# Performance work log

Measured on AMD Instinct MI355X. Metric: run time of the kernel, lower is better.

## Reference

```python
import jax, jax.numpy as jnp
import numpy as np

B, N, D, H = 4, 4096, 1024, 16
DH = D // H          # per-head dim = 64
M = 256              # number of random features
KEPS = 1e-3          # performer kernel epsilon
LNEPS = 1e-5


def setup_inputs() -> dict:
    key = jax.random.key(0)
    ks = jax.random.split(key, 16)
    s = 0.02
    return {
        "src": jax.random.normal(ks[0], (B, N, D), jnp.float32),
        "Wq": s * jax.random.normal(ks[1], (D, D), jnp.float32),
        "Wk": s * jax.random.normal(ks[2], (D, D), jnp.float32),
        "Wv": s * jax.random.normal(ks[3], (D, D), jnp.float32),
        "Wout": s * jax.random.normal(ks[4], (D, D), jnp.float32),
        "b_out": jnp.zeros((D,), jnp.float32),
        "proj": jax.random.normal(ks[5], (M, DH), jnp.float32),
        "g1": jnp.ones((D,), jnp.float32),
        "beta1": jnp.zeros((D,), jnp.float32),
        "W1": s * jax.random.normal(ks[6], (2048, D), jnp.float32),
        "b1": jnp.zeros((2048,), jnp.float32),
        "W2": s * jax.random.normal(ks[7], (D, 2048), jnp.float32),
        "b2": jnp.zeros((D,), jnp.float32),
        "g2": jnp.ones((D,), jnp.float32),
        "beta2": jnp.zeros((D,), jnp.float32),
    }


def _layernorm(x, g, b):
    mu = x.mean(-1, keepdims=True)
    var = ((x - mu) ** 2).mean(-1, keepdims=True)
    return (x - mu) * jax.lax.rsqrt(var + LNEPS) * g + b


def _softmax_kernel(x, proj, is_query):
    # FAVOR+ positive softmax kernel feature map (performer_pytorch)
    dn = DH ** -0.25           # data normalizer d^{-1/4}
    ratio = M ** -0.5
    data_dash = jnp.einsum('bhnd,md->bhnm', x * dn, proj)
    diag = (x ** 2).sum(-1) * 0.5 * dn * dn            # [b,h,n]
    if is_query:
        stab = data_dash.max(-1, keepdims=True)
    else:
        stab = data_dash.max()
    return ratio * (jnp.exp(data_dash - diag[..., None] - stab) + KEPS)


def reference(src, Wq, Wk, Wv, Wout, b_out, proj, g1, beta1, W1, b1, W2, b2, g2, beta2):
    # ---- Performer self-attention (FAVOR+, non-causal) ----
    def split_heads(x):
        return x.reshape(B, N, H, DH).transpose(0, 2, 1, 3)  # [b,h,n,dh]

    q = split_heads(src @ Wq.T)
    k = split_heads(src @ Wk.T)
    v = split_heads(src @ Wv.T)

    qp = _softmax_kernel(q, proj, is_query=True)   # [b,h,n,m]
    kp = _softmax_kernel(k, proj, is_query=False)  # [b,h,n,m]

    k_sum = kp.sum(-2)                                        # [b,h,m]
    d_inv = 1.0 / jnp.einsum('bhnm,bhm->bhn', qp, k_sum)      # [b,h,n]
    context = jnp.einsum('bhnm,bhnd->bhmd', kp, v)            # [b,h,m,dh]
    attn = jnp.einsum('bhnm,bhmd->bhnd', qp, context) * d_inv[..., None]

    attn = attn.transpose(0, 2, 1, 3).reshape(B, N, D)
    src2 = attn @ Wout.T + b_out

    # ---- residual + norm + FFN (dropout = identity at eval) ----
    x = _layernorm(src + src2, g1, beta1)
    ff = (jax.nn.gelu(x @ W1.T + b1, approximate=False)) @ W2.T + b2
    return _layernorm(x + ff, g2, beta2)
```

## Files before the change

kernel.cpp:

```cpp
#include <hip/hip_runtime.h>

#define DEVI __device__ __forceinline__

using u16 = unsigned short;
using u32 = unsigned int;
using u64 = unsigned long long;

typedef __bf16 bf16x8 __attribute__((ext_vector_type(8)));
typedef float  f32x4  __attribute__((ext_vector_type(4)));

constexpr int BB = 4, NN = 4096, DD = 1024, HH = 16, DH = 64, MF = 256;
constexpr int RT = BB * NN;
constexpr int QKVS = 3072;
constexpr float DN    = 0.35355339059327373f;
constexpr float RATIO = 0.0625f;
constexpr float DIAGC = 0.0625f;
constexpr float KEPSC = 1e-3f;

DEVI u16 f2bf(float f) {
  u32 u = __float_as_uint(f);
  u32 r = u + 0x7fffu + ((u >> 16) & 1u);
  return (u16)(r >> 16);
}
DEVI float bf2f(u16 u) { return __uint_as_float(((u32)u) << 16); }

typedef void __attribute__((address_space(1)))* gas1;
typedef void __attribute__((address_space(3)))* las3;
DEVI void gload_lds16(const void* g, void* l) {
  __builtin_amdgcn_global_load_lds((gas1)(u64)g, (las3)(u32)(u64)l, 16, 0, 0);
}

DEVI bf16x8 ldswz(const u16* base, int row, int kbyte) {
  int p = (row << 7) + kbyte;
  p ^= (row & 7) << 4;
  return *(const bf16x8*)((const char*)base + p);
}

__global__ void cast_kernel(const float* __restrict__ in, u16* __restrict__ out, int n4) {
  int i = blockIdx.x * 256 + threadIdx.x;
  int stride = gridDim.x * 256;
  for (; i < n4; i += stride) {
    float4 v = ((const float4*)in)[i];
    ushort4 o; o.x = f2bf(v.x); o.y = f2bf(v.y); o.z = f2bf(v.z); o.w = f2bf(v.w);
    ((ushort4*)out)[i] = o;
  }
}

__global__ void cast_weights_kernel(
    const float* __restrict__ Wq, const float* __restrict__ Wk,
    const float* __restrict__ Wv, const float* __restrict__ Wout,
    const float* __restrict__ W1, const float* __restrict__ W2,
    const float* __restrict__ proj,
    u16* __restrict__ wqkvb, u16* __restrict__ wob,
    u16* __restrict__ w1b, u16* __restrict__ w2b, u16* __restrict__ projb)
{
  constexpr int TOT = 2101248;
  int i = blockIdx.x * 256 + threadIdx.x;
  const int stride = gridDim.x * 256;
  for (; i < TOT; i += stride) {
    const float* s; u16* d; int loc; float sc = 1.0f;
    if (i < 1048576) {
      int seg = i >> 18; loc = i & 262143;
      s = (seg == 0) ? Wq : (seg == 1) ? Wk : (seg == 2) ? Wv : Wout;
      d = (seg < 3) ? (wqkvb + seg * 1048576) : wob;
    } else if (i < 1572864) { loc = i - 1048576; s = W1; d = w1b; }
    else if (i < 2097152)   { loc = i - 1572864; s = W2; d = w2b; }
    else                    { loc = i - 2097152; s = proj; d = projb; sc = DN; }
    float4 v = ((const float4*)s)[loc];
    ushort4 o; o.x = f2bf(v.x * sc); o.y = f2bf(v.y * sc); o.z = f2bf(v.z * sc); o.w = f2bf(v.w * sc);
    ((ushort4*)d)[loc] = o;
  }
}

template <int EPI>
__global__ __launch_bounds__(512, 4) void gemm_bt(
    const u16* __restrict__ A, int lda, const u16* __restrict__ Bm,
    u16* __restrict__ Cb, const float* __restrict__ bias,
    int Ncols, int K)
{
  __shared__ __align__(16) u16 sA[256 * 64];
  __shared__ __align__(16) u16 sB[128 * 64];
  const int tid = threadIdx.x, lane = tid & 63;
  const int wv = tid >> 6, wr = wv >> 1, wc = wv & 1;

  const int gx = gridDim.x;
  const int wg = blockIdx.y * gx + blockIdx.x;
  const int cpx = (gx * gridDim.y) >> 3;
  const int swz = (wg & 7) * cpx + (wg >> 3);
  const int bn = swz % gx, bm = swz / gx;

  f32x4 acc[4][4] = {};

  int rowS[4], colS[4], ldsb[4];
#pragma unroll
  for (int it = 0; it < 4; ++it) {
    int p = (it * 512 + tid) * 16;
    ldsb[it] = (it * 512 + (tid & ~63)) * 16;
    int sp = p ^ (((p >> 7) & 7) << 4);
    rowS[it] = sp >> 7;
    colS[it] = (sp >> 1) & 63;
  }
  const size_t baseA = (size_t)bm * 256, baseB = (size_t)bn * 128;

  for (int kt = 0; kt < K; kt += 64) {
#pragma unroll
    for (int it = 0; it < 4; ++it)
      gload_lds16(A + (baseA + rowS[it]) * lda + kt + colS[it], (char*)sA + ldsb[it]);
#pragma unroll
    for (int it = 0; it < 2; ++it)
      gload_lds16(Bm + (baseB + rowS[it]) * K + kt + colS[it], (char*)sB + ldsb[it]);
    __syncthreads();
#pragma unroll
    for (int kk = 0; kk < 2; ++kk) {
      const int kbyte = kk * 64 + ((lane >> 4) << 4);
      bf16x8 a[4], b[4];
#pragma unroll
      for (int i = 0; i < 4; ++i) a[i] = ldswz(sA, wr * 64 + i * 16 + (lane & 15), kbyte);
#pragma unroll
      for (int i = 0; i < 4; ++i) b[i] = ldswz(sB, wc * 64 + i * 16 + (lane & 15), kbyte);
#pragma unroll
      for (int i = 0; i < 4; ++i)
#pragma unroll
        for (int j = 0; j < 4; ++j)
          acc[i][j] = __builtin_amdgcn_mfma_f32_16x16x32_bf16(a[i], b[j], acc[i][j], 0, 0, 0);
    }
    __syncthreads();
  }

#pragma unroll
  for (int i = 0; i < 4; ++i) {
    const int gr0 = bm * 256 + wr * 64 + i * 16 + ((lane >> 4) << 2);
#pragma unroll
    for (int j = 0; j < 4; ++j) {
      const int gc = bn * 128 + wc * 64 + j * 16 + (lane & 15);
#pragma unroll
      for (int r = 0; r < 4; ++r) {
        const size_t o = (size_t)(gr0 + r) * Ncols + gc;
        const float v = acc[i][j][r];
        if constexpr (EPI == 0) {
          Cb[o] = f2bf(v);
        } else if constexpr (EPI == 2) {
          float t = v + bias[gc];
          Cb[o] = f2bf(0.5f * t * (1.0f + erff(t * 0.70710678118654752f)));
        } else {
          Cb[o] = f2bf(v + bias[gc]);
        }
      }
    }
  }
}

__global__ __launch_bounds__(256) void kmax_kernel(
    const u16* __restrict__ qkvb, const u16* __restrict__ projb, float* __restrict__ pmax)
{
  __shared__ __align__(16) u16 sX[64 * 72];
  __shared__ float sred[4];
  const int tid = threadIdx.x, lane = tid & 63, wv = tid >> 6;
  const int bh = blockIdx.x, b = bh >> 4, h = bh & 15;
  const int n0 = blockIdx.y * 64;

  for (int i = tid; i < 512; i += 256) {
    int r = i >> 3, c8 = (i & 7) << 3;
    uint4 v = *(const uint4*)(qkvb + ((size_t)(b * NN + n0 + r)) * QKVS + 1024 + h * DH + c8);
    *(uint4*)&sX[r * 72 + c8] = v;
  }
  __syncthreads();

  f32x4 dacc[16] = {};
#pragma unroll
  for (int kk = 0; kk < 2; ++kk) {
    const int ko = kk * 32 + ((lane >> 4) << 3);
    bf16x8 a = *(const bf16x8*)&sX[(wv * 16 + (lane & 15)) * 72 + ko];
#pragma unroll
    for (int f = 0; f < 16; ++f) {
      bf16x8 bb = *(const bf16x8*)(projb + (f * 16 + (lane & 15)) * 64 + ko);
      dacc[f] = __builtin_amdgcn_mfma_f32_16x16x32_bf16(a, bb, dacc[f], 0, 0, 0);
    }
  }
  float mx = -1e30f;
#pragma unroll
  for (int f = 0; f < 16; ++f)
#pragma unroll
    for (int r = 0; r < 4; ++r) mx = fmaxf(mx, dacc[f][r]);
#pragma unroll
  for (int m = 1; m < 64; m <<= 1) mx = fmaxf(mx, __shfl_xor(mx, m));
  if (lane == 0) sred[wv] = mx;
  __syncthreads();
  if (tid == 0)
    pmax[blockIdx.y * gridDim.x + blockIdx.x] =
        fmaxf(fmaxf(sred[0], sred[1]), fmaxf(sred[2], sred[3]));
}

__global__ __launch_bounds__(256) void reduce_max_kernel(
    const float* __restrict__ pmax, float* __restrict__ stab)
{
  const int tid = threadIdx.x;
  float mx = -1e30f;
#pragma unroll
  for (int i = 0; i < 16; ++i) mx = fmaxf(mx, pmax[i * 256 + tid]);
#pragma unroll
  for (int m = 1; m < 64; m <<= 1) mx = fmaxf(mx, __shfl_xor(mx, m));
  __shared__ float sred[4];
  if ((tid & 63) == 0) sred[tid >> 6] = mx;
  __syncthreads();
  if (tid == 0)
    stab[0] = fmaxf(fmaxf(sred[0], sred[1]), fmaxf(sred[2], sred[3]));
}

__global__ __launch_bounds__(256, 1) void kctx_kernel(
    const u16* __restrict__ qkvb, const u16* __restrict__ projb,
    const float* __restrict__ stab_p,
    float* __restrict__ ctxT, float* __restrict__ ksum)
{
  __shared__ __align__(16) u16 sX[64 * 72];
  __shared__ __align__(16) u16 sVT[64 * 72];
  __shared__ __align__(16) u16 sKpT[256 * 72];
  __shared__ float sDiag[64];
  const int tid = threadIdx.x, lane = tid & 63, wv = tid >> 6;
  const int bh = blockIdx.x, b = bh >> 4, h = bh & 15;
  const int sl = blockIdx.y;
  const float stab = stab_p[0];

  f32x4 cacc[16] = {};
  float ksacc[16] = {};
  const int row_base = wv * 16 + ((lane >> 4) << 2);

  for (int t = 0; t < 8; ++t) {
    const int n0 = sl * 512 + t * 64;
    if (t) __syncthreads();
    for (int i = tid; i < 512; i += 256) {
      int r = i >> 3, c8 = (i & 7) << 3;
      size_t g = ((size_t)(b * NN + n0 + r)) * QKVS + h * DH + c8;
      uint4 xv = *(const uint4*)(qkvb + g + 1024);
      *(uint4*)&sX[r * 72 + c8] = xv;
      uint4 vv = *(const uint4*)(qkvb + g + 2048);
      const u16* pv = (const u16*)&vv;
#pragma unroll
      for (int j = 0; j < 8; ++j) sVT[(c8 + j) * 72 + r] = pv[j];
    }
    __syncthreads();
    {
      int r = tid >> 2, qq = tid & 3;
      float s = 0;
#pragma unroll
      for (int j = 0; j < 16; ++j) { float x = bf2f(sX[r * 72 + qq * 16 + j]); s += x * x; }
      s += __shfl_xor(s, 1); s += __shfl_xor(s, 2);
      if (qq == 0) sDiag[r] = DIAGC * s;
    }
    f32x4 dacc[16] = {};
#pragma unroll
    for (int kk = 0; kk < 2; ++kk) {
      const int ko = kk * 32 + ((lane >> 4) << 3);
      bf16x8 a = *(const bf16x8*)&sX[(wv * 16 + (lane & 15)) * 72 + ko];
#pragma unroll
      for (int f = 0; f < 16; ++f) {
        bf16x8 bb = *(const bf16x8*)(projb + (f * 16 + (lane & 15)) * 64 + ko);
        dacc[f] = __builtin_amdgcn_mfma_f32_16x16x32_bf16(a, bb, dacc[f], 0, 0, 0);
      }
    }
    __syncthreads();
#pragma unroll
    for (int f = 0; f < 16; ++f) {
      float kvv[4]; float cs = 0;
#pragma unroll
      for (int r = 0; r < 4; ++r) {
        float val = RATIO * (__expf(dacc[f][r] - sDiag[row_base + r] - stab) + KEPSC);
        kvv[r] = val; cs += val;
      }
      cs += __shfl_xor(cs, 16); cs += __shfl_xor(cs, 32);
      ksacc[f] += cs;
      ushort4 pk; pk.x = f2bf(kvv[0]); pk.y = f2bf(kvv[1]); pk.z = f2bf(kvv[2]); pk.w = f2bf(kvv[3]);
      *(ushort4*)&sKpT[(f * 16 + (lane & 15)) * 72 + row_base] = pk;
    }
    __syncthreads();
#pragma unroll
    for (int kk = 0; kk < 2; ++kk) {
      const int ko = kk * 32 + ((lane >> 4) << 3);
      bf16x8 a = *(const bf16x8*)&sVT[(wv * 16 + (lane & 15)) * 72 + ko];
#pragma unroll
      for (int f = 0; f < 16; ++f) {
        bf16x8 bb = *(const bf16x8*)&sKpT[(f * 16 + (lane & 15)) * 72 + ko];
        cacc[f] = __builtin_amdgcn_mfma_f32_16x16x32_bf16(a, bb, cacc[f], 0, 0, 0);
      }
    }
  }
#pragma unroll
  for (int f = 0; f < 16; ++f) {
    const int m = f * 16 + (lane & 15);
#pragma unroll
    for (int r = 0; r < 4; ++r)
      atomicAdd(&ctxT[((size_t)bh * 64 + row_base + r) * 256 + m], cacc[f][r]);
  }
  if (lane < 16) {
#pragma unroll
    for (int f = 0; f < 16; ++f) atomicAdd(&ksum[bh * 256 + f * 16 + lane], ksacc[f]);
  }
}

__global__ __launch_bounds__(256) void ctxfin_kernel(
    const float* __restrict__ ctxT, u16* __restrict__ ctxb)
{
  const int i = blockIdx.x * 256 + threadIdx.x;
  float4 v = ((const float4*)ctxT)[i];
  ushort4 o; o.x = f2bf(v.x); o.y = f2bf(v.y); o.z = f2bf(v.z); o.w = f2bf(v.w);
  ((ushort4*)ctxb)[i] = o;
}

__global__ __launch_bounds__(256, 2) void qattn_kernel(
    u16* qkvb, const u16* __restrict__ projb,
    const u16* __restrict__ ctxb, const float* __restrict__ ksum)
{
  __shared__ __align__(16) u16 sCtx[64 * 256];
  __shared__ __align__(16) u16 sX[64 * 72];
  __shared__ __align__(16) u16 sQp[64 * 264];
  __shared__ float sKsum[256];
  __shared__ float sDiag[64];
  __shared__ float sDinv[64];
  const int tid = threadIdx.x, lane = tid & 63, wv = tid >> 6;
  const int bh = blockIdx.x, b = bh >> 4, h = bh & 15;

  {
    const char* cbase = (const char*)(ctxb + (size_t)bh * 16384);
#pragma unroll
    for (int it = 0; it < 8; ++it) {
      int p = (it * 256 + tid) * 16;
      int ldsb = (it * 256 + (tid & ~63)) * 16;
      int q = p ^ (((p >> 9) & 7) << 4);
      gload_lds16(cbase + q, (char*)sCtx + ldsb);
    }
  }
  sKsum[tid] = ksum[bh * 256 + tid];

  const int row_base = wv * 16 + ((lane >> 4) << 2);
  const int wr = wv >> 1, wc = wv & 1;

  for (int rt = 0; rt < 2; ++rt) {
    const int n0 = (blockIdx.y * 2 + rt) * 64;
    for (int i = tid; i < 512; i += 256) {
      int r = i >> 3, c8 = (i & 7) << 3;
      uint4 v = *(const uint4*)(qkvb + ((size_t)(b * NN + n0 + r)) * QKVS + h * DH + c8);
      *(uint4*)&sX[r * 72 + c8] = v;
    }
    __syncthreads();
    {
      int r = tid >> 2, qq = tid & 3;
      float s = 0;
#pragma unroll
      for (int j = 0; j < 16; ++j) { float x = bf2f(sX[r * 72 + qq * 16 + j]); s += x * x; }
      s += __shfl_xor(s, 1); s += __shfl_xor(s, 2);
      if (qq == 0) sDiag[r] = DIAGC * s;
    }
    f32x4 dacc[16] = {};
#pragma unroll
    for (int kk = 0; kk < 2; ++kk) {
      const int ko = kk * 32 + ((lane >> 4) << 3);
      bf16x8 a = *(const bf16x8*)&sX[(wv * 16 + (lane & 15)) * 72 + ko];
#pragma unroll
      for (int f = 0; f < 16; ++f) {
        bf16x8 bb = *(const bf16x8*)(projb + (f * 16 + (lane & 15)) * 64 + ko);
        dacc[f] = __builtin_amdgcn_mfma_f32_16x16x32_bf16(a, bb, dacc[f], 0, 0, 0);
      }
    }
    __syncthreads();
#pragma unroll
    for (int r = 0; r < 4; ++r) {
      const int row = row_base + r;
      float mx = dacc[0][r];
#pragma unroll
      for (int f = 1; f < 16; ++f) mx = fmaxf(mx, dacc[f][r]);
      mx = fmaxf(mx, __shfl_xor(mx, 1));
      mx = fmaxf(mx, __shfl_xor(mx, 2));
      mx = fmaxf(mx, __shfl_xor(mx, 4));
      mx = fmaxf(mx, __shfl_xor(mx, 8));
      const float dg = sDiag[row];
      float ds = 0;
#pragma unroll
      for (int f = 0; f < 16; ++f) {
        float qv = RATIO * (__expf(dacc[f][r] - dg - mx) + KEPSC);
        dacc[f][r] = qv;
        ds += qv * sKsum[f * 16 + (lane & 15)];
      }
      ds += __shfl_xor(ds, 1); ds += __shfl_xor(ds, 2);
      ds += __shfl_xor(ds, 4); ds += __shfl_xor(ds, 8);
      if ((lane & 15) == 0) sDinv[row] = 1.0f / ds;
    }
#pragma unroll
    for (int f = 0; f < 16; ++f)
#pragma unroll
      for (int r = 0; r < 4; ++r)
        sQp[(row_base + r) * 264 + f * 16 + (lane & 15)] = f2bf(dacc[f][r]);
    __syncthreads();

    f32x4 acc2[2][2] = {};
#pragma unroll
    for (int kk = 0; kk < 8; ++kk) {
      const int koe = kk * 32 + ((lane >> 4) << 3);
      const int kob = koe * 2;
      bf16x8 a0 = *(const bf16x8*)&sQp[(wr * 32 + (lane & 15)) * 264 + koe];
      bf16x8 a1 = *(const bf16x8*)&sQp[(wr * 32 + 16 + (lane & 15)) * 264 + koe];
      const int j0 = wc * 32 + (lane & 15), j1 = j0 + 16;
      bf16x8 b0 = *(const bf16x8*)((const char*)sCtx + (((j0 << 9) + kob) ^ ((j0 & 7) << 4)));
      bf16x8 b1 = *(const bf16x8*)((const char*)sCtx + (((j1 << 9) + kob) ^ ((j1 & 7) << 4)));
      acc2[0][0] = __builtin_amdgcn_mfma_f32_16x16x32_bf16(a0, b0, acc2[0][0], 0, 0, 0);
      acc2[0][1] = __builtin_amdgcn_mfma_f32_16x16x32_bf16(a0, b1, acc2[0][1], 0, 0, 0);
      acc2[1][0] = __builtin_amdgcn_mfma_f32_16x16x32_bf16(a1, b0, acc2[1][0], 0, 0, 0);
      acc2[1][1] = __builtin_amdgcn_mfma_f32_16x16x32_bf16(a1, b1, acc2[1][1], 0, 0, 0);
    }
#pragma unroll
    for (int mi = 0; mi < 2; ++mi)
#pragma unroll
      for (int ni = 0; ni < 2; ++ni)
#pragma unroll
        for (int r = 0; r < 4; ++r) {
          const int row = wr * 32 + mi * 16 + ((lane >> 4) << 2) + r;
          const int col = wc * 32 + ni * 16 + (lane & 15);
          float v = acc2[mi][ni][r] * sDinv[row];
          qkvb[((size_t)(b * NN + n0 + row)) * QKVS + h * DH + col] = f2bf(v);
        }
    __syncthreads();
  }
}

__global__ __launch_bounds__(256) void ln1_kernel(
    const float* __restrict__ src, const u16* __restrict__ wout,
    const float* __restrict__ g, const float* __restrict__ be, u16* __restrict__ xb)
{
  const int row = blockIdx.x, tid = threadIdx.x;
  const float4 sv = ((const float4*)(src + (size_t)row * DD))[tid];
  const ushort4 wv = ((const ushort4*)(wout + (size_t)row * DD))[tid];
  float x0 = sv.x + bf2f(wv.x);
  float x1 = sv.y + bf2f(wv.y);
  float x2 = sv.z + bf2f(wv.z);
  float x3 = sv.w + bf2f(wv.w);
  float s = x0 + x1 + x2 + x3;
  float ss = x0 * x0 + x1 * x1 + x2 * x2 + x3 * x3;
#pragma unroll
  for (int m = 1; m < 64; m <<= 1) { s += __shfl_xor(s, m); ss += __shfl_xor(ss, m); }
  __shared__ float red[8];
  if ((tid & 63) == 0) { red[tid >> 6] = s; red[4 + (tid >> 6)] = ss; }
  __syncthreads();
  s = red[0] + red[1] + red[2] + red[3];
  ss = red[4] + red[5] + red[6] + red[7];
  const float mu = s * (1.0f / DD);
  const float rs = rsqrtf(ss * (1.0f / DD) - mu * mu + 1e-5f);
  const float4 gv = ((const float4*)g)[tid];
  const float4 bv = ((const float4*)be)[tid];
  ushort4 o;
  o.x = f2bf((x0 - mu) * rs * gv.x + bv.x);
  o.y = f2bf((x1 - mu) * rs * gv.y + bv.y);
  o.z = f2bf((x2 - mu) * rs * gv.z + bv.z);
  o.w = f2bf((x3 - mu) * rs * gv.w + bv.w);
  ((ushort4*)(xb + (size_t)row * DD))[tid] = o;
}

__global__ __launch_bounds__(256) void ln2_kernel(
    const u16* __restrict__ xb, const u16* __restrict__ ff,
    const float* __restrict__ g, const float* __restrict__ be, float* __restrict__ out)
{
  const int row = blockIdx.x, tid = threadIdx.x;
  const ushort4 xv = ((const ushort4*)(xb + (size_t)row * DD))[tid];
  const ushort4 fv = ((const ushort4*)(ff + (size_t)row * DD))[tid];
  float x0 = bf2f(xv.x) + bf2f(fv.x);
  float x1 = bf2f(xv.y) + bf2f(fv.y);
  float x2 = bf2f(xv.z) + bf2f(fv.z);
  float x3 = bf2f(xv.w) + bf2f(fv.w);
  float s = x0 + x1 + x2 + x3;
  float ss = x0 * x0 + x1 * x1 + x2 * x2 + x3 * x3;
#pragma unroll
  for (int m = 1; m < 64; m <<= 1) { s += __shfl_xor(s, m); ss += __shfl_xor(ss, m); }
  __shared__ float red[8];
  if ((tid & 63) == 0) { red[tid >> 6] = s; red[4 + (tid >> 6)] = ss; }
  __syncthreads();
  s = red[0] + red[1] + red[2] + red[3];
  ss = red[4] + red[5] + red[6] + red[7];
  const float mu = s * (1.0f / DD);
  const float rs = rsqrtf(ss * (1.0f / DD) - mu * mu + 1e-5f);
  const float4 gv = ((const float4*)g)[tid];
  const float4 bv = ((const float4*)be)[tid];
  float4 o;
  o.x = (x0 - mu) * rs * gv.x + bv.x;
  o.y = (x1 - mu) * rs * gv.y + bv.y;
  o.z = (x2 - mu) * rs * gv.z + bv.z;
  o.w = (x3 - mu) * rs * gv.w + bv.w;
  ((float4*)(out + (size_t)row * DD))[tid] = o;
}

extern "C" void kernel_launch(void* const* d_in, const int* in_sizes, int n_in,
                              void* d_out, int out_size, void* d_ws, size_t ws_size,
                              hipStream_t stream) {
  (void)in_sizes; (void)n_in; (void)out_size; (void)ws_size;
  const float* src   = (const float*)d_in[0];
  const float* Wq    = (const float*)d_in[1];
  const float* Wk    = (const float*)d_in[2];
  const float* Wv    = (const float*)d_in[3];
  const float* Wout  = (const float*)d_in[4];
  const float* b_out = (const float*)d_in[5];
  const float* proj  = (const float*)d_in[6];
  const float* g1    = (const float*)d_in[7];
  const float* be1   = (const float*)d_in[8];
  const float* W1    = (const float*)d_in[9];
  const float* b1    = (const float*)d_in[10];
  const float* W2    = (const float*)d_in[11];
  const float* b2    = (const float*)d_in[12];
  const float* g2    = (const float*)d_in[13];
  const float* be2   = (const float*)d_in[14];

  char* ws = (char*)d_ws;
  constexpr size_t OFF_SRCB = 0;
  constexpr size_t OFF_QKV  = 33554432;
  constexpr size_t OFF_XB   = 67108864;
  constexpr size_t OFF_WOUTB= 100663296;
  constexpr size_t OFF_WQKV = 134217728;
  constexpr size_t OFF_WO   = 140509184;
  constexpr size_t OFF_W1   = 142606336;
  constexpr size_t OFF_W2   = 146800640;
  constexpr size_t OFF_PROJ = 150994944;
  constexpr size_t OFF_CTXT = 151027712;
  constexpr size_t OFF_KSUM = 155222016;
  constexpr size_t OFF_PMAX = 155287552;
  constexpr size_t OFF_STAB = 155303936;

  u16* srcb  = (u16*)(ws + OFF_SRCB);
  u16* qkvb  = (u16*)(ws + OFF_QKV);
  u16* wqkvb = (u16*)(ws + OFF_WQKV);
  u16* wob   = (u16*)(ws + OFF_WO);
  u16* w1b   = (u16*)(ws + OFF_W1);
  u16* w2b   = (u16*)(ws + OFF_W2);
  u16* projb = (u16*)(ws + OFF_PROJ);
  float* ctxT = (float*)(ws + OFF_CTXT);
  float* ksum = (float*)(ws + OFF_KSUM);
  float* pmax = (float*)(ws + OFF_PMAX);
  float* stab = (float*)(ws + OFF_STAB);
  u16* ctxb  = (u16*)(ws + OFF_SRCB);
  u16* woutb = (u16*)(ws + OFF_WOUTB);
  u16* xb    = (u16*)(ws + OFF_XB);
  u16* h1    = (u16*)(ws + OFF_SRCB);
  u16* ff    = (u16*)(ws + OFF_WOUTB);

  cast_kernel<<<4096, 256, 0, stream>>>(src, srcb, RT * DD / 4);
  cast_weights_kernel<<<2048, 256, 0, stream>>>(Wq, Wk, Wv, Wout, W1, W2, proj,
                                                wqkvb, wob, w1b, w2b, projb);
  hipMemsetAsync(ws + OFF_CTXT, 0, 4194304 + 65536, stream);

  gemm_bt<0><<<dim3(QKVS / 128, RT / 256), 512, 0, stream>>>(srcb, DD, wqkvb, qkvb, nullptr, QKVS, DD);

  kmax_kernel<<<dim3(64, 64), 256, 0, stream>>>(qkvb, projb, pmax);
  reduce_max_kernel<<<1, 256, 0, stream>>>(pmax, stab);
  kctx_kernel<<<dim3(64, 8), 256, 0, stream>>>(qkvb, projb, stab, ctxT, ksum);
  ctxfin_kernel<<<4096, 256, 0, stream>>>(ctxT, ctxb);
  qattn_kernel<<<dim3(64, 32), 256, 0, stream>>>(qkvb, projb, ctxb, ksum);

  gemm_bt<3><<<dim3(DD / 128, RT / 256), 512, 0, stream>>>(qkvb, QKVS, wob, woutb, b_out, DD, DD);
  ln1_kernel<<<RT, 256, 0, stream>>>(src, woutb, g1, be1, xb);

  gemm_bt<2><<<dim3(2048 / 128, RT / 256), 512, 0, stream>>>(xb, DD, w1b, h1, b1, 2048, DD);
  gemm_bt<3><<<dim3(DD / 128, RT / 256), 512, 0, stream>>>(h1, 2048, w2b, ff, b2, DD, 2048);
  ln2_kernel<<<RT, 256, 0, stream>>>(xb, ff, g2, be2, (float*)d_out);
}
```

Measured before the change: 721.3 us.

## Split kctx feature dimension across blocks and fuse diag into load

Splits the 256 random features of kctx_kernel into two halves handled by separate blocks, doubling the grid to 1024 blocks and halving per-block registers and shared memory so launch bounds can target 4 blocks per CU. The diagonal norm is now computed from registers during the tile load, removing a shared-memory pass and one barrier. V is stored transposed with a stride of 68 to change the bank pattern and is read back as two 4-element halves. The cost is that each K tile and V tile is loaded and transposed twice, once per half, and the number of atomics stays the same in total.

```diff
diff --git a/kernel.cpp b/kernel.cpp
--- a/kernel.cpp
+++ b/kernel.cpp
@@ -7,6 +7,7 @@
 using u64 = unsigned long long;
 
 typedef __bf16 bf16x8 __attribute__((ext_vector_type(8)));
+typedef __bf16 bf16x4 __attribute__((ext_vector_type(4)));
 typedef float  f32x4  __attribute__((ext_vector_type(4)));
 
 constexpr int BB = 4, NN = 4096, DD = 1024, HH = 16, DH = 64, MF = 256;
@@ -207,60 +208,62 @@
     stab[0] = fmaxf(fmaxf(sred[0], sred[1]), fmaxf(sred[2], sred[3]));
 }
 
-__global__ __launch_bounds__(256, 1) void kctx_kernel(
+__global__ __launch_bounds__(256, 4) void kctx_kernel(
     const u16* __restrict__ qkvb, const u16* __restrict__ projb,
     const float* __restrict__ stab_p,
     float* __restrict__ ctxT, float* __restrict__ ksum)
 {
   __shared__ __align__(16) u16 sX[64 * 72];
-  __shared__ __align__(16) u16 sVT[64 * 72];
-  __shared__ __align__(16) u16 sKpT[256 * 72];
+  __shared__ __align__(16) u16 sVT[64 * 68];
+  __shared__ __align__(16) u16 sKpT[128 * 72];
   __shared__ float sDiag[64];
   const int tid = threadIdx.x, lane = tid & 63, wv = tid >> 6;
   const int bh = blockIdx.x, b = bh >> 4, h = bh & 15;
-  const int sl = blockIdx.y;
+  const int sl = blockIdx.y >> 1, mh = blockIdx.y & 1;
   const float stab = stab_p[0];
 
-  f32x4 cacc[16] = {};
-  float ksacc[16] = {};
+  f32x4 cacc[8] = {};
+  float ksacc[8] = {};
   const int row_base = wv * 16 + ((lane >> 4) << 2);
 
   for (int t = 0; t < 8; ++t) {
     const int n0 = sl * 512 + t * 64;
     if (t) __syncthreads();
-    for (int i = tid; i < 512; i += 256) {
+#pragma unroll
+    for (int it = 0; it < 2; ++it) {
+      int i = it * 256 + tid;
       int r = i >> 3, c8 = (i & 7) << 3;
       size_t g = ((size_t)(b * NN + n0 + r)) * QKVS + h * DH + c8;
       uint4 xv = *(const uint4*)(qkvb + g + 1024);
       *(uint4*)&sX[r * 72 + c8] = xv;
+      {
+        const u16* px = (const u16*)&xv;
+        float s = 0;
+#pragma unroll
+        for (int j = 0; j < 8; ++j) { float x = bf2f(px[j]); s += x * x; }
+        s += __shfl_xor(s, 1); s += __shfl_xor(s, 2); s += __shfl_xor(s, 4);
+        if ((tid & 7) == 0) sDiag[r] = DIAGC * s;
+      }
       uint4 vv = *(const uint4*)(qkvb + g + 2048);
       const u16* pv = (const u16*)&vv;
 #pragma unroll
-      for (int j = 0; j < 8; ++j) sVT[(c8 + j) * 72 + r] = pv[j];
-    }
-    __syncthreads();
-    {
-      int r = tid >> 2, qq = tid & 3;
-      float s = 0;
-#pragma unroll
-      for (int j = 0; j < 16; ++j) { float x = bf2f(sX[r * 72 + qq * 16 + j]); s += x * x; }
-      s += __shfl_xor(s, 1); s += __shfl_xor(s, 2);
-      if (qq == 0) sDiag[r] = DIAGC * s;
-    }
-    f32x4 dacc[16] = {};
+      for (int j = 0; j < 8; ++j) sVT[(c8 + j) * 68 + r] = pv[j];
+    }
+    __syncthreads();
+
+    f32x4 dacc[8] = {};
 #pragma unroll
     for (int kk = 0; kk < 2; ++kk) {
       const int ko = kk * 32 + ((lane >> 4) << 3);
       bf16x8 a = *(const bf16x8*)&sX[(wv * 16 + (lane & 15)) * 72 + ko];
 #pragma unroll
-      for (int f = 0; f < 16; ++f) {
-        bf16x8 bb = *(const bf16x8*)(projb + (f * 16 + (lane & 15)) * 64 + ko);
+      for (int f = 0; f < 8; ++f) {
+        bf16x8 bb = *(const bf16x8*)(projb + (mh * 128 + f * 16 + (lane & 15)) * 64 + ko);
         dacc[f] = __builtin_amdgcn_mfma_f32_16x16x32_bf16(a, bb, dacc[f], 0, 0, 0);
       }
     }
-    __syncthreads();
-#pragma unroll
-    for (int f = 0; f < 16; ++f) {
+#pragma unroll
+    for (int f = 0; f < 8; ++f) {
       float kvv[4]; float cs = 0;
 #pragma unroll
       for (int r = 0; r < 4; ++r) {
@@ -276,24 +279,30 @@
 #pragma unroll
     for (int kk = 0; kk < 2; ++kk) {
       const int ko = kk * 32 + ((lane >> 4) << 3);
-      bf16x8 a = *(const bf16x8*)&sVT[(wv * 16 + (lane & 15)) * 72 + ko];
-#pragma unroll
-      for (int f = 0; f < 16; ++f) {
+      const int vrow = wv * 16 + (lane & 15);
+      bf16x4 lo = *(const bf16x4*)&sVT[vrow * 68 + ko];
+      bf16x4 hi = *(const bf16x4*)&sVT[vrow * 68 + ko + 4];
+      bf16x8 a;
+#pragma unroll
+      for (int e = 0; e < 4; ++e) { a[e] = lo[e]; a[e + 4] = hi[e]; }
+#pragma unroll
+      for (int f = 0; f < 8; ++f) {
         bf16x8 bb = *(const bf16x8*)&sKpT[(f * 16 + (lane & 15)) * 72 + ko];
         cacc[f] = __builtin_amdgcn_mfma_f32_16x16x32_bf16(a, bb, cacc[f], 0, 0, 0);
       }
     }
   }
 #pragma unroll
-  for (int f = 0; f < 16; ++f) {
-    const int m = f * 16 + (lane & 15);
+  for (int f = 0; f < 8; ++f) {
+    const int m = mh * 128 + f * 16 + (lane & 15);
 #pragma unroll
     for (int r = 0; r < 4; ++r)
       atomicAdd(&ctxT[((size_t)bh * 64 + row_base + r) * 256 + m], cacc[f][r]);
   }
   if (lane < 16) {
 #pragma unroll
-    for (int f = 0; f < 16; ++f) atomicAdd(&ksum[bh * 256 + f * 16 + lane], ksacc[f]);
+    for (int f = 0; f < 8; ++f)
+      atomicAdd(&ksum[bh * 256 + mh * 128 + f * 16 + lane], ksacc[f]);
   }
 }
 
@@ -546,7 +555,7 @@
 
   kmax_kernel<<<dim3(64, 64), 256, 0, stream>>>(qkvb, projb, pmax);
   reduce_max_kernel<<<1, 256, 0, stream>>>(pmax, stab);
-  kctx_kernel<<<dim3(64, 8), 256, 0, stream>>>(qkvb, projb, stab, ctxT, ksum);
+  kctx_kernel<<<dim3(64, 16), 256, 0, stream>>>(qkvb, projb, stab, ctxT, ksum);
   ctxfin_kernel<<<4096, 256, 0, stream>>>(ctxT, ctxb);
   qattn_kernel<<<dim3(64, 32), 256, 0, stream>>>(qkvb, projb, ctxb, ksum);
 
```

After: 739.2 us. +2.5%, slower.
